# Performance work log

Measured on AMD Instinct MI355X. Metric: run time of the kernel, lower is better.

## Reference

```python
import jax, jax.numpy as jnp
import numpy as np

LATENT, ACTION, HIDDEN, TEMB = 256, 32, 1024, 128
BATCH, NTRAJ, HORIZON = 1024, 16, 5
EPI_W, PRAG_W, CONS_W, GAMMA = 1.0, 1.0, 0.1, 0.99
LOG2PI = float(np.log(2.0 * np.pi))


def _dense_init(key, fan_in, fan_out):
    return jax.random.normal(key, (fan_in, fan_out), dtype=jnp.float32) / np.sqrt(fan_in)


def time_embed(t):
    # sinusoidal embedding, TEMB dims, like ValueNetwork(time_embed_dim=128)
    half = TEMB // 2
    freqs = jnp.exp(-np.log(10000.0) * jnp.arange(half, dtype=jnp.float32) / half)
    ang = t[:, None] * freqs[None, :]  # [B, half]
    return jnp.concatenate([jnp.sin(ang), jnp.cos(ang)], axis=-1)  # [B, TEMB]


def setup_inputs() -> dict:
    key = jax.random.key(0)
    ks = jax.random.split(key, 12)
    return {
        "latent": jax.random.normal(ks[0], (BATCH, LATENT), dtype=jnp.float32),
        "noise": jax.random.normal(ks[1], (NTRAJ, HORIZON, BATCH, ACTION), dtype=jnp.float32),
        # DiffusionConditionedPolicy (state-dependent std): trunk + mean/log_std heads
        "pW1": _dense_init(ks[2], LATENT, HIDDEN), "pb1": jnp.zeros((HIDDEN,), jnp.float32),
        "pW2": _dense_init(ks[3], HIDDEN, HIDDEN), "pb2": jnp.zeros((HIDDEN,), jnp.float32),
        "pWm": _dense_init(ks[4], HIDDEN, ACTION), "pbm": jnp.zeros((ACTION,), jnp.float32),
        "pWs": _dense_init(ks[5], HIDDEN, ACTION), "pbs": jnp.zeros((ACTION,), jnp.float32),
        # LatentDynamicsModel: 3-layer MLP on [latent, action] -> delta
        "dW1": _dense_init(ks[6], LATENT + ACTION, HIDDEN), "db1": jnp.zeros((HIDDEN,), jnp.float32),
        "dW2": _dense_init(ks[7], HIDDEN, HIDDEN), "db2": jnp.zeros((HIDDEN,), jnp.float32),
        "dW3": _dense_init(ks[8], HIDDEN, LATENT), "db3": jnp.zeros((LATENT,), jnp.float32),
        # ValueNetwork: 3-layer MLP on [latent, time_embed] -> scalar
        "vW1": _dense_init(ks[9], LATENT + TEMB, HIDDEN), "vb1": jnp.zeros((HIDDEN,), jnp.float32),
        "vW2": _dense_init(ks[10], HIDDEN, HIDDEN), "vb2": jnp.zeros((HIDDEN,), jnp.float32),
        "vW3": _dense_init(ks[11], HIDDEN, 1), "vb3": jnp.zeros((1,), jnp.float32),
    }


def _efe_forward(latent, noise, pW1, pb1, pW2, pb2, pWm, pbm, pWs, pbs,
                 dW1, db1, dW2, db2, dW3, db3, vW1, vb1, vW2, vb2, vW3, vb3):
    def policy(z, eps):
        h = jax.nn.silu(z @ pW1 + pb1)
        h = jax.nn.silu(h @ pW2 + pb2)
        mean = h @ pWm + pbm
        log_std = jnp.clip(h @ pWs + pbs, -5.0, 2.0)
        action = mean + jnp.exp(log_std) * eps  # reparameterized sample
        # Normal entropy per-dim, summed over action dim
        ent = jnp.sum(0.5 * (1.0 + LOG2PI) + log_std, axis=-1)
        return action, ent

    def dynamics(z, a):
        h = jnp.concatenate([z, a], axis=-1)
        h = jax.nn.silu(h @ dW1 + db1)
        h = jax.nn.silu(h @ dW2 + db2)
        return h @ dW3 + db3  # delta latent

    def value(z, tvec):
        h = jnp.concatenate([z, time_embed(tvec)], axis=-1)
        h = jax.nn.silu(h @ vW1 + vb1)
        h = jax.nn.silu(h @ vW2 + vb2)
        return (h @ vW3 + vb3)[..., 0]  # squeeze(-1)

    def step(z, inp):
        eps_t, t = inp
        action, ent = policy(z, eps_t)
        z_next = z + dynamics(z, action)  # predict_next_latent
        # _compute_latent_kl on normalized latents
        zn = z / (jnp.linalg.norm(z, axis=-1, keepdims=True) + 1e-8)
        pn = z_next / (jnp.linalg.norm(z_next, axis=-1, keepdims=True) + 1e-8)
        kl = 0.5 * jnp.sum((zn - pn) ** 2, axis=-1)
        epistemic = jnp.log1p(kl)
        tvec = jnp.full((z.shape[0],), 0.0, dtype=z.dtype) + t
        pragmatic = value(z_next, tvec)
        consistency = -ent
        step_efe = EPI_W * epistemic + PRAG_W * pragmatic + CONS_W * consistency
        return z_next, step_efe

    ts = jnp.arange(HORIZON, dtype=jnp.float32)

    def rollout(eps_traj):  # eps_traj: [H, B, A]
        _, efes = jax.lax.scan(step, latent, (eps_traj, ts))  # efes: [H, B]
        disc = GAMMA ** ts  # discount_factor ** t
        return jnp.sum(disc[:, None] * efes, axis=0)  # traj_efe: [B]

    traj_efe = jax.vmap(rollout)(noise)  # [NTRAJ, B]
    total_efe = jnp.mean(traj_efe, axis=0)  # sum of traj_efe / num_trajectories
    return total_efe


def reference(latent, noise, pW1, pb1, pW2, pb2, pWm, pbm, pWs, pbs,
              dW1, db1, dW2, db2, dW3, db3, vW1, vb1, vW2, vb2, vW3, vb3):
    return _efe_forward(latent, noise, pW1, pb1, pW2, pb2, pWm, pbm, pWs, pbs,
                        dW1, db1, dW2, db2, dW3, db3, vW1, vb1, vW2, vb2, vW3, vb3)
```

## Files before the change

kernel.cpp:

```cpp
#include <hip/hip_runtime.h>
#include <cstdint>
#include <cstddef>
#include <cmath>


typedef __bf16 bf16;
typedef __attribute__((ext_vector_type(8))) __bf16 bf16x8;
typedef __attribute__((ext_vector_type(4))) __bf16 bf16x4;
typedef __attribute__((ext_vector_type(4))) float f32x4;

static constexpr int BATCH = 1024, NTRAJ = 16, HORIZON = 5;
static constexpr int MR = NTRAJ * BATCH;
static constexpr float ENT_C = 1.4189385332046727f;
static constexpr float SUMDISC = 4.90099501f;

__device__ __forceinline__ void gld_lds16(const bf16* g, const bf16* l) {
  typedef __attribute__((address_space(1))) const uint32_t gq_t;
  typedef __attribute__((address_space(3))) uint32_t lq_t;
  gq_t* gp = (gq_t*)(uintptr_t)g;
  lq_t* lp = (lq_t*)(uint32_t)(uintptr_t)l;
  __builtin_amdgcn_global_load_lds(gp, lp, 16, 0, 0);
}

__device__ __forceinline__ float silu(float x) {
  return x * __builtin_amdgcn_rcpf(1.f + __expf(-x));
}

#define MFMA16(a, b, c) __builtin_amdgcn_mfma_f32_16x16x32_bf16((a), (b), (c), 0, 0, 0)
#define SBAR() __builtin_amdgcn_s_barrier()
#define SCHED0() __builtin_amdgcn_sched_barrier(0)
#define VMCNT(n) asm volatile("s_waitcnt vmcnt(" #n ")" ::: "memory")
#define LGKMCNT0() asm volatile("s_waitcnt lgkmcnt(0)" ::: "memory")

__global__ __launch_bounds__(256) void gemm128(
    const bf16* __restrict__ A, int lda, int K, const bf16* __restrict__ Bt,
    const float* __restrict__ bias, int act_cols,
    bf16* __restrict__ C1, bf16* __restrict__ C2, int ldc) {
  __shared__ alignas(16) bf16 PA[2][2][128 * 32];
  __shared__ alignas(16) bf16 PB[2][2][128 * 32];
  const int tid = threadIdx.x, wave = tid >> 6, lane = tid & 63;
  const int quad = lane >> 4, l16 = lane & 15;
  const int rowBlk = blockIdx.x * 128, colBlk = blockIdx.y * 128;
  const int wr = wave >> 1, wc = wave & 1;
  const int srow = lane >> 2;
  const int skel = (((lane & 3) ^ ((lane >> 3) & 3)) * 8);
  const int qsw = quad ^ ((l16 >> 1) & 3);

  const bf16* gA0 = A + (size_t)(rowBlk + wave * 32 + srow) * lda + skel;
  const bf16* gA1 = gA0 + (size_t)16 * lda;
  const bf16* gB0 = Bt + (size_t)(colBlk + wave * 32 + srow) * K + skel;
  const bf16* gB1 = gB0 + (size_t)16 * K;

#define STG128(t, b)                                      \
  do {                                                    \
    const int k0_ = (t)*64;                               \
    gld_lds16(gA0 + k0_, &PA[b][0][wave * 1024]);         \
    gld_lds16(gA1 + k0_, &PA[b][0][wave * 1024 + 512]);   \
    gld_lds16(gA0 + k0_ + 32, &PA[b][1][wave * 1024]);    \
    gld_lds16(gA1 + k0_ + 32, &PA[b][1][wave * 1024 + 512]); \
    gld_lds16(gB0 + k0_, &PB[b][0][wave * 1024]);         \
    gld_lds16(gB1 + k0_, &PB[b][0][wave * 1024 + 512]);   \
    gld_lds16(gB0 + k0_ + 32, &PB[b][1][wave * 1024]);    \
    gld_lds16(gB1 + k0_ + 32, &PB[b][1][wave * 1024 + 512]); \
  } while (0)

  f32x4 acc[4][4] = {};
  const int nt = K >> 6;
  STG128(0, 0);
  STG128(1, 1);
  VMCNT(8);
  SBAR();
  SCHED0();
  for (int t = 0; t < nt; ++t) {
    const int b = t & 1;
#pragma unroll
    for (int ks = 0; ks < 2; ++ks) {
      const bf16* aRd = &PA[b][ks][(wr * 64 + l16) * 32 + qsw * 8];
      const bf16* bRd = &PB[b][ks][(wc * 64 + l16) * 32 + qsw * 8];
      bf16x8 af[4], bfr[4];
#pragma unroll
      for (int i = 0; i < 4; ++i) {
        af[i] = *(const bf16x8*)(aRd + i * 16 * 32);
        bfr[i] = *(const bf16x8*)(bRd + i * 16 * 32);
      }
#pragma unroll
      for (int mi = 0; mi < 4; ++mi)
#pragma unroll
        for (int ni = 0; ni < 4; ++ni)
          acc[mi][ni] = MFMA16(bfr[ni], af[mi], acc[mi][ni]);
    }
    if (t == nt - 1) break;
    SBAR();
    SCHED0();
    if (t + 2 < nt) {
      STG128(t + 2, b);
      VMCNT(8);
    } else {
      VMCNT(0);
    }
    SBAR();
    SCHED0();
  }
#undef STG128

  const bool doAct = (colBlk < act_cols);
  bf16* const Cp = doAct ? C1 : C2;
  const int cShift = doAct ? 0 : act_cols;
#pragma unroll
  for (int mi = 0; mi < 4; ++mi) {
    const int row = rowBlk + wr * 64 + mi * 16 + l16;
#pragma unroll
    for (int ni = 0; ni < 4; ++ni) {
      const int col0 = colBlk + wc * 64 + ni * 16 + quad * 4;
      const f32x4 bb = *(const f32x4*)(bias + col0);
      bf16x4 o;
#pragma unroll
      for (int r = 0; r < 4; ++r) {
        float x = acc[mi][ni][r] + bb[r];
        if (doAct) x = silu(x);
        o[r] = (bf16)x;
      }
      *(bf16x4*)(Cp + (size_t)row * ldc + (col0 - cShift)) = o;
    }
  }
}

__global__ __launch_bounds__(256) void gemm_pd1v(
    const bf16* __restrict__ A, const bf16* __restrict__ Bt,
    const float* __restrict__ pdb1, const float* __restrict__ vbiasT,
    bf16* __restrict__ Ha, bf16* __restrict__ Hp, bf16* __restrict__ Hv) {
  __shared__ alignas(16) bf16 As0[128 * 32], As1[128 * 32];
  __shared__ alignas(16) bf16 Bs0[128 * 32], Bs1[128 * 32];
  const int tid = threadIdx.x, wave = tid >> 6, lane = tid & 63;
  const int quad = lane >> 4, l16 = lane & 15;
  const int rowBlk = blockIdx.x * 128, colBlk = blockIdx.y * 128;
  const int wr = wave >> 1, wc = wave & 1;
  const int srow = lane >> 2;
  const int skel = (((lane & 3) ^ ((lane >> 3) & 3)) * 8);
  const int qsw = quad ^ ((l16 >> 1) & 3);

  const bf16* gA0 = A + (size_t)(rowBlk + wave * 32 + srow) * 256 + skel;
  const bf16* gA1 = gA0 + (size_t)16 * 256;
  const bf16* gB0 = Bt + (size_t)(colBlk + wave * 32 + srow) * 256 + skel;
  const bf16* gB1 = gB0 + (size_t)16 * 256;
  bf16* const lA0 = As0 + wave * 32 * 32;
  bf16* const lA0b = As0 + (wave * 32 + 16) * 32;
  bf16* const lA1 = As1 + wave * 32 * 32;
  bf16* const lA1b = As1 + (wave * 32 + 16) * 32;
  bf16* const lB0 = Bs0 + wave * 32 * 32;
  bf16* const lB0b = Bs0 + (wave * 32 + 16) * 32;
  bf16* const lB1 = Bs1 + wave * 32 * 32;
  bf16* const lB1b = Bs1 + (wave * 32 + 16) * 32;

  f32x4 acc[4][4] = {};
  for (int k0 = 0; k0 < 256; k0 += 64) {
    gld_lds16(gA0 + k0, lA0);
    gld_lds16(gA1 + k0, lA0b);
    gld_lds16(gA0 + k0 + 32, lA1);
    gld_lds16(gA1 + k0 + 32, lA1b);
    gld_lds16(gB0 + k0, lB0);
    gld_lds16(gB1 + k0, lB0b);
    gld_lds16(gB0 + k0 + 32, lB1);
    gld_lds16(gB1 + k0 + 32, lB1b);
    __syncthreads();
#pragma unroll
    for (int ks = 0; ks < 2; ++ks) {
      const bf16* aRd = (ks ? As1 : As0) + (wr * 64 + l16) * 32 + qsw * 8;
      const bf16* bRd = (ks ? Bs1 : Bs0) + (wc * 64 + l16) * 32 + qsw * 8;
      bf16x8 af[4], bfr[4];
#pragma unroll
      for (int i = 0; i < 4; ++i) {
        af[i] = *(const bf16x8*)(aRd + i * 16 * 32);
        bfr[i] = *(const bf16x8*)(bRd + i * 16 * 32);
      }
#pragma unroll
      for (int mi = 0; mi < 4; ++mi)
#pragma unroll
        for (int ni = 0; ni < 4; ++ni)
          acc[mi][ni] = MFMA16(bfr[ni], af[mi], acc[mi][ni]);
    }
    __syncthreads();
  }

  const int seg = colBlk >> 10;
  bf16* const Cp = (seg == 0) ? Ha : (seg == 1) ? Hp : Hv;
  const int cShift = seg << 10;
  const float* const bp = (seg == 2) ? (vbiasT - 2048) : pdb1;
#pragma unroll
  for (int mi = 0; mi < 4; ++mi) {
    const int row = rowBlk + wr * 64 + mi * 16 + l16;
#pragma unroll
    for (int ni = 0; ni < 4; ++ni) {
      const int col0 = colBlk + wc * 64 + ni * 16 + quad * 4;
      const f32x4 bb = *(const f32x4*)(bp + col0);
      bf16x4 o;
#pragma unroll
      for (int r = 0; r < 4; ++r) {
        float x = acc[mi][ni][r] + bb[r];
        if (seg != 1) x = silu(x);
        o[r] = (bf16)x;
      }
      *(bf16x4*)(Cp + (size_t)row * 1024 + (col0 - cShift)) = o;
    }
  }
}

template <int NT, int EPI>
__device__ __forceinline__ void gemm256_body(
    const bf16* __restrict__ A, const bf16* __restrict__ Bt, int rowBlk,
    int colBlk, const float* __restrict__ bias, const float* __restrict__ aux,
    bf16* __restrict__ C1, float* __restrict__ efe, float disc,
    bf16 (*sAB)[2][256 * 64]) {
  constexpr int K = NT * 64;
  const int tid = threadIdx.x, wave = tid >> 6, lane = tid & 63;
  const int quad = lane >> 4, l16 = lane & 15;
  const int wr = wave >> 2, wc = wave & 3;

  const int j8 = lane >> 3;
  const int c16e = ((lane & 7) ^ j8) * 8;
  const bf16* gAs = A + (size_t)(rowBlk + wave * 16 + j8) * K + c16e;
  const bf16* gBs = Bt + (size_t)(colBlk + wave * 16 + j8) * K + c16e;

#define STAGE_A(hh, tt, bb)                                           \
  do {                                                                \
    const bf16* g_ = gAs + (hh) * 128 * K + (tt) * 64;                \
    bf16* l_ = &sAB[(bb)][0][((hh) * 128 + wave * 16) * 64];          \
    gld_lds16(g_, l_);                                                \
    gld_lds16(g_ + 8 * K, l_ + 8 * 64);                               \
  } while (0)
#define STAGE_B(hh, tt, bb)                                           \
  do {                                                                \
    const bf16* g_ = gBs + (hh) * 128 * K + (tt) * 64;                \
    bf16* l_ = &sAB[(bb)][1][((hh) * 128 + wave * 16) * 64];          \
    gld_lds16(g_, l_);                                                \
    gld_lds16(g_ + 8 * K, l_ + 8 * 64);                               \
  } while (0)

  const int k0x = (quad * 8) ^ ((l16 & 7) << 3);
  const int aOff = (wr * 128 + l16) * 64 + k0x;
  const int bOff = (wc * 64 + l16) * 64 + k0x;

  bf16x8 bAf[4][2], bBf[2][2], bB2f[2][2];
  f32x4 acc[8][4] = {};

  STAGE_A(0, 0, 0);
  STAGE_A(1, 0, 0);
  STAGE_B(0, 0, 0);
  STAGE_B(1, 0, 0);
  STAGE_B(0, 1, 1);
  STAGE_B(1, 1, 1);
  VMCNT(4);
  SBAR();
  SCHED0();

#pragma unroll 2
  for (int t = 0; t < NT; ++t) {
    const int buf = t & 1;
    const bf16* lA = &sAB[buf][0][0];
    const bf16* lB = &sAB[buf][1][0];

#pragma unroll
    for (int m = 0; m < 4; ++m)
#pragma unroll
      for (int ks = 0; ks < 2; ++ks)
        bAf[m][ks] = *(const bf16x8*)(lA + ((aOff + m * 1024) ^ (ks << 5)));
#pragma unroll
    for (int n = 0; n < 2; ++n)
#pragma unroll
      for (int ks = 0; ks < 2; ++ks)
        bBf[n][ks] = *(const bf16x8*)(lB + ((bOff + n * 1024) ^ (ks << 5)));
    if (t + 1 < NT) STAGE_A(0, t + 1, buf ^ 1);
    SBAR();
    LGKMCNT0();
    SCHED0();
    __builtin_amdgcn_s_setprio(1);
#pragma unroll
    for (int ks = 0; ks < 2; ++ks)
#pragma unroll
      for (int m = 0; m < 4; ++m)
#pragma unroll
        for (int n = 0; n < 2; ++n)
          acc[m][n] = MFMA16(bBf[n][ks], bAf[m][ks], acc[m][n]);
    __builtin_amdgcn_s_setprio(0);
    SBAR();
    SCHED0();

#pragma unroll
    for (int n = 0; n < 2; ++n)
#pragma unroll
      for (int ks = 0; ks < 2; ++ks)
        bB2f[n][ks] =
            *(const bf16x8*)(lB + ((bOff + (n + 2) * 1024) ^ (ks << 5)));
    if (t + 1 < NT) STAGE_A(1, t + 1, buf ^ 1);
    SBAR();
    LGKMCNT0();
    SCHED0();
    __builtin_amdgcn_s_setprio(1);
#pragma unroll
    for (int ks = 0; ks < 2; ++ks)
#pragma unroll
      for (int m = 0; m < 4; ++m)
#pragma unroll
        for (int n = 0; n < 2; ++n)
          acc[m][n + 2] = MFMA16(bB2f[n][ks], bAf[m][ks], acc[m][n + 2]);
    __builtin_amdgcn_s_setprio(0);
    SBAR();
    SCHED0();

#pragma unroll
    for (int m = 0; m < 4; ++m)
#pragma unroll
      for (int ks = 0; ks < 2; ++ks)
        bAf[m][ks] =
            *(const bf16x8*)(lA + ((aOff + (m + 4) * 1024) ^ (ks << 5)));
    if (t + 2 < NT) STAGE_B(0, t + 2, buf);
    SBAR();
    LGKMCNT0();
    SCHED0();
    __builtin_amdgcn_s_setprio(1);
#pragma unroll
    for (int ks = 0; ks < 2; ++ks)
#pragma unroll
      for (int m = 0; m < 4; ++m)
#pragma unroll
        for (int n = 0; n < 2; ++n)
          acc[m + 4][n + 2] =
              MFMA16(bB2f[n][ks], bAf[m][ks], acc[m + 4][n + 2]);
    __builtin_amdgcn_s_setprio(0);
    SBAR();
    SCHED0();

    if (t + 2 < NT) STAGE_B(1, t + 2, buf);
    SBAR();
    SCHED0();
    __builtin_amdgcn_s_setprio(1);
#pragma unroll
    for (int ks = 0; ks < 2; ++ks)
#pragma unroll
      for (int m = 0; m < 4; ++m)
#pragma unroll
        for (int n = 0; n < 2; ++n)
          acc[m + 4][n] = MFMA16(bBf[n][ks], bAf[m][ks], acc[m + 4][n]);
    __builtin_amdgcn_s_setprio(0);
    if (t < NT - 2) {
      VMCNT(4);
    } else {
      VMCNT(0);
    }
    SBAR();
    SCHED0();
  }
#undef STAGE_A
#undef STAGE_B

  if constexpr (EPI == 0) {
#pragma unroll
    for (int m = 0; m < 8; ++m) {
      const int row = rowBlk + wr * 128 + m * 16 + l16;
#pragma unroll
      for (int n = 0; n < 4; ++n) {
        const int gcol = colBlk + wc * 64 + n * 16 + quad * 4;
        const f32x4 bb = *(const f32x4*)(bias + gcol);
        bf16x4 o;
#pragma unroll
        for (int r = 0; r < 4; ++r) o[r] = (bf16)silu(acc[m][n][r] + bb[r]);
        *(bf16x4*)(C1 + (size_t)row * 1024 + gcol) = o;
      }
    }
  } else {
#pragma unroll
    for (int m = 0; m < 8; ++m) {
      const int row = rowBlk + wr * 128 + m * 16 + l16;
      float p = 0.f;
#pragma unroll
      for (int n = 0; n < 4; ++n) {
        const int gcol = colBlk + wc * 64 + n * 16 + quad * 4;
        const f32x4 bb = *(const f32x4*)(bias + gcol);
        const f32x4 w3 = *(const f32x4*)(aux + gcol);
#pragma unroll
        for (int r = 0; r < 4; ++r) p += silu(acc[m][n][r] + bb[r]) * w3[r];
      }
      p += __shfl_xor(p, 16);
      p += __shfl_xor(p, 32);
      if (quad == 0) atomicAdd(efe + row, disc * p);
    }
  }
}

template <int NT, int EPI>
__global__ __launch_bounds__(512, 2) void gemm256(
    const bf16* __restrict__ A, const bf16* __restrict__ Bt, int nCol,
    const float* __restrict__ bias, const float* __restrict__ aux,
    bf16* __restrict__ C1, float* __restrict__ efe, float disc) {
  static_assert(NT >= 2, "need at least 2 K-tiles");
  __shared__ alignas(16) bf16 sAB[2][2][256 * 64];
  const int nwg = gridDim.x, flat = blockIdx.x;
  const int lid = (flat & 7) * (nwg >> 3) + (flat >> 3);
  const int rowBlk = (lid / nCol) * 256, colBlk = (lid % nCol) * 256;
  gemm256_body<NT, EPI>(A, Bt, rowBlk, colBlk, bias, aux, C1, efe, disc, sAB);
}

template <int NT>
__global__ __launch_bounds__(512, 2) void gemm256_dual(
    const bf16* __restrict__ A0, const bf16* __restrict__ Bt0,
    const float* __restrict__ bias0, bf16* __restrict__ C0,
    const bf16* __restrict__ A1, const bf16* __restrict__ Bt1,
    const float* __restrict__ bias1, const float* __restrict__ aux1,
    float* __restrict__ efe, float disc) {
  __shared__ alignas(16) bf16 sAB[2][2][256 * 64];
  const int nwg = gridDim.x, flat = blockIdx.x;
  const int lid = (flat & 7) * (nwg >> 3) + (flat >> 3);
  const int job = lid >> 8;
  const int t256 = lid & 255;
  const int rowBlk = (t256 >> 2) * 256, colBlk = (t256 & 3) * 256;
  if (job == 0)
    gemm256_body<NT, 0>(A0, Bt0, rowBlk, colBlk, bias0, nullptr, C0, nullptr,
                        0.f, sAB);
  else
    gemm256_body<NT, 1>(A1, Bt1, rowBlk, colBlk, bias1, aux1, nullptr, efe,
                        disc, sAB);
}

__global__ __launch_bounds__(256) void gemm_dyn3(
    const bf16* __restrict__ A, const bf16* __restrict__ Bt,
    const float* __restrict__ db3, float* __restrict__ Zf,
    bf16* __restrict__ Zb, float* __restrict__ s_n, float* __restrict__ s_c) {
  __shared__ alignas(16) bf16 PA[2][2][64 * 32];
  __shared__ alignas(16) bf16 PB[2][2][128 * 32];
  const int tid = threadIdx.x, wave = tid >> 6, lane = tid & 63;
  const int quad = lane >> 4, l16 = lane & 15;
  const int rowBlk = blockIdx.x * 64, colBlk = blockIdx.y * 128;
  const int srow = lane >> 2;
  const int skel = (((lane & 3) ^ ((lane >> 3) & 3)) * 8);
  const int qsw = quad ^ ((l16 >> 1) & 3);

  const bf16* gA = A + (size_t)(rowBlk + wave * 16 + srow) * 1024 + skel;
  const bf16* gB0 = Bt + (size_t)(colBlk + wave * 32 + srow) * 1024 + skel;
  const bf16* gB1 = gB0 + (size_t)16 * 1024;

#define STGD(t, b)                                        \
  do {                                                    \
    const int k0_ = (t)*64;                               \
    gld_lds16(gA + k0_, &PA[b][0][wave * 512]);           \
    gld_lds16(gA + k0_ + 32, &PA[b][1][wave * 512]);      \
    gld_lds16(gB0 + k0_, &PB[b][0][wave * 1024]);         \
    gld_lds16(gB1 + k0_, &PB[b][0][wave * 1024 + 512]);   \
    gld_lds16(gB0 + k0_ + 32, &PB[b][1][wave * 1024]);    \
    gld_lds16(gB1 + k0_ + 32, &PB[b][1][wave * 1024 + 512]); \
  } while (0)

  f32x4 acc[8] = {};
  STGD(0, 0);
  STGD(1, 1);
  VMCNT(6);
  SBAR();
  SCHED0();
#pragma unroll 2
  for (int t = 0; t < 16; ++t) {
    const int b = t & 1;
#pragma unroll
    for (int ks = 0; ks < 2; ++ks) {
      const bf16* aRd = &PA[b][ks][(wave * 16 + l16) * 32 + qsw * 8];
      const bf16* bRd = &PB[b][ks][l16 * 32 + qsw * 8];
      const bf16x8 af = *(const bf16x8*)aRd;
#pragma unroll
      for (int ni = 0; ni < 8; ++ni) {
        const bf16x8 bfr = *(const bf16x8*)(bRd + ni * 16 * 32);
        acc[ni] = MFMA16(bfr, af, acc[ni]);
      }
    }
    if (t == 15) break;
    SBAR();
    SCHED0();
    if (t < 14) {
      STGD(t + 2, b);
      VMCNT(6);
    } else {
      VMCNT(0);
    }
    SBAR();
    SCHED0();
  }
#undef STGD

  const int row = rowBlk + wave * 16 + l16;
  float pn = 0.f, pc = 0.f;
#pragma unroll
  for (int ni = 0; ni < 8; ++ni) {
    const int col0 = colBlk + ni * 16 + quad * 4;
    const f32x4 b4 = *(const f32x4*)(db3 + col0);
    float* zp = Zf + (size_t)row * 256 + col0;
    const f32x4 z = *(const f32x4*)zp;
    f32x4 zn;
    bf16x4 o;
#pragma unroll
    for (int r = 0; r < 4; ++r) {
      zn[r] = z[r] + acc[ni][r] + b4[r];
      pn += zn[r] * zn[r];
      pc += z[r] * zn[r];
      o[r] = (bf16)zn[r];
    }
    *(f32x4*)zp = zn;
    *(bf16x4*)(Zb + (size_t)row * 256 + col0) = o;
  }
  pn += __shfl_xor(pn, 16);
  pn += __shfl_xor(pn, 32);
  pc += __shfl_xor(pc, 16);
  pc += __shfl_xor(pc, 32);
  if (quad == 0) {
    atomicAdd(s_n + row, pn);
    atomicAdd(s_c + row, pc);
  }
}

__global__ void kl_batch(const float* __restrict__ sz0,
                         const float* __restrict__ snAll,
                         const float* __restrict__ scAll,
                         float* __restrict__ efe) {
  const int m = blockIdx.x * 256 + threadIdx.x;
  float sz = sz0[m];
  float disc = 1.f, acc = 0.f;
  for (int t = 0; t < HORIZON; ++t) {
    const float sn = snAll[t * MR + m], sc = scAll[t * MR + m];
    const float nz = sqrtf(sz) + 1e-8f, nn = sqrtf(sn) + 1e-8f;
    const float kl =
        0.5f * (sz / (nz * nz) + sn / (nn * nn) - 2.f * sc / (nz * nn));
    acc += disc * log1pf(fmaxf(kl, 0.f));
    sz = sn;
    disc *= 0.99f;
  }
  efe[m] += acc;
}

__global__ __launch_bounds__(256) void heads4(
    const bf16* __restrict__ H, const bf16* __restrict__ Wt,
    const float* __restrict__ pbm, const float* __restrict__ pbs,
    const float* __restrict__ noise, const bf16* __restrict__ preD,
    const bf16* __restrict__ dW1at, bf16* __restrict__ Hd,
    float* __restrict__ efe, int t, float disc, int rmask) {
  __shared__ alignas(16) bf16 As[2][4 * 16 * 32];
  __shared__ alignas(16) bf16 Bs[2][4 * 64 * 32];
  __shared__ alignas(16) bf16 LAct[16 * 32];
  const int tid = threadIdx.x, wave = tid >> 6, lane = tid & 63;
  const int quad = lane >> 4, l16 = lane & 15;
  const int rowBlk = blockIdx.x * 16;
  const int srow = lane >> 2;
  const int skel = (((lane & 3) ^ ((lane >> 3) & 3)) * 8);
  const int qsw = quad ^ ((l16 >> 1) & 3);
  const int kw = wave * 256;

  const bf16* gA = H + (size_t)((rowBlk + srow) & rmask) * 1024 + kw + skel;

#define STGH(kt, b)                                                         \
  do {                                                                      \
    gld_lds16(gA + (kt) * 32, &As[b][wave * 512]);                          \
    _Pragma("unroll") for (int j = 0; j < 4; ++j) gld_lds16(                \
        Wt + (size_t)(j * 16 + srow) * 1024 + kw + (kt) * 32 + skel,        \
        &Bs[b][wave * 2048 + j * 512]);                                     \
  } while (0)

  f32x4 acc[4] = {};
  STGH(0, 0);
  STGH(1, 1);
#pragma unroll
  for (int kt = 0; kt < 8; ++kt) {
    const int b = kt & 1;
    if (kt < 7) {
      VMCNT(5);
    } else {
      VMCNT(0);
    }
    SCHED0();
    const bf16x8 af =
        *(const bf16x8*)(&As[b][wave * 512] + l16 * 32 + qsw * 8);
#pragma unroll
    for (int ni = 0; ni < 4; ++ni) {
      const bf16x8 bfr =
          *(const bf16x8*)(&Bs[b][wave * 2048] + (ni * 16 + l16) * 32 + qsw * 8);
      acc[ni] = MFMA16(bfr, af, acc[ni]);
    }
    SCHED0();
    if (kt < 6) {
      LGKMCNT0();
      STGH(kt + 2, b);
    }
  }
#undef STGH

  float* red = (float*)Bs;
#pragma unroll
  for (int ni = 0; ni < 4; ++ni)
    *(f32x4*)(red + wave * 1024 + ni * 256 + lane * 4) = acc[ni];
  __syncthreads();
#pragma unroll
  for (int ni = 0; ni < 4; ++ni) {
    f32x4 s = *(const f32x4*)(red + ni * 256 + lane * 4);
#pragma unroll
    for (int w2 = 1; w2 < 4; ++w2) {
      const f32x4 p = *(const f32x4*)(red + w2 * 1024 + ni * 256 + lane * 4);
#pragma unroll
      for (int r = 0; r < 4; ++r) s[r] += p[r];
    }
    acc[ni] = s;
  }

  const int row = rowBlk + l16;
  const int n = row >> 10, b2 = row & 1023;
  float ent = 0.f;
#pragma unroll
  for (int ni = 0; ni < 2; ++ni) {
    const int col0 = ni * 16 + quad * 4;
    const f32x4 bm4 = *(const f32x4*)(pbm + col0);
    const f32x4 bs4 = *(const f32x4*)(pbs + col0);
    const f32x4 ep4 =
        *(const f32x4*)(noise + (((size_t)(n * 5 + t) * 1024 + b2) * 32 + col0));
    bf16x4 o;
#pragma unroll
    for (int r = 0; r < 4; ++r) {
      const float mean = acc[ni][r] + bm4[r];
      float ls = acc[ni + 2][r] + bs4[r];
      ls = fminf(fmaxf(ls, -5.f), 2.f);
      o[r] = (bf16)(mean + __expf(ls) * ep4[r]);
      ent += ENT_C + ls;
    }
    if (wave == 0) *(bf16x4*)(LAct + l16 * 32 + col0) = o;
  }
  ent += __shfl_xor(ent, 16);
  ent += __shfl_xor(ent, 32);
  if (wave == 0 && quad == 0) efe[row] += disc * (-0.1f) * ent;
  __syncthreads();

  const int prow = row & rmask;
  const bf16x8 af2 = *(const bf16x8*)(LAct + l16 * 32 + quad * 8);
#pragma unroll 4
  for (int ci = 0; ci < 16; ++ci) {
    const int ct = wave * 16 + ci;
    const bf16x8 wf =
        *(const bf16x8*)(dW1at + (size_t)(ct * 16 + l16) * 32 + quad * 8);
    f32x4 a = {};
    a = MFMA16(wf, af2, a);
    const int col0 = ct * 16 + quad * 4;
    const bf16x4 pd = *(const bf16x4*)(preD + (size_t)prow * 1024 + col0);
    bf16x4 o;
#pragma unroll
    for (int r = 0; r < 4; ++r) o[r] = (bf16)silu(a[r] + (float)pd[r]);
    *(bf16x4*)(Hd + (size_t)row * 1024 + col0) = o;
  }
}

__global__ __launch_bounds__(256) void prep_tr(
    const float* __restrict__ pW1, const float* __restrict__ dW1,
    const float* __restrict__ vW1, const float* __restrict__ pW2,
    const float* __restrict__ dW2, const float* __restrict__ dW3,
    const float* __restrict__ vW2, const float* __restrict__ pWm,
    const float* __restrict__ pWs, const float* __restrict__ pb1,
    const float* __restrict__ db1, const float* __restrict__ vb1,
    const float* __restrict__ latent, bf16* __restrict__ pdW1vt,
    bf16* __restrict__ pW2t, bf16* __restrict__ pHt,
    bf16* __restrict__ dW1at, bf16* __restrict__ dW2t,
    bf16* __restrict__ dW3t, bf16* __restrict__ vW2t,
    float* __restrict__ pdb1, float* __restrict__ vbias,
    float* __restrict__ Zf, bf16* __restrict__ Zb0, float* __restrict__ efe,
    float* __restrict__ sz0, float* __restrict__ snAll,
    float* __restrict__ scAll) {
  int bid = blockIdx.x;
  if (bid == 1072) {
    for (int i = threadIdx.x; i < 2048; i += 256)
      pdb1[i] = (i < 1024) ? pb1[i] : db1[i - 1024];
    return;
  }
  if (bid >= 1073 && bid < 1093) {
    const int idx = (bid - 1073) * 256 + threadIdx.x;
    const int t = idx >> 10, j = idx & 1023;
    float s = vb1[j];
    const float lt = (float)t;
    for (int i = 0; i < 64; ++i) {
      const float f = expf(-9.210340371976184f * (float)i / 64.f);
      const float ang = lt * f;
      s += sinf(ang) * vW1[(size_t)(256 + i) * 1024 + j];
      s += cosf(ang) * vW1[(size_t)(256 + 64 + i) * 1024 + j];
    }
    vbias[idx] = s;
    return;
  }
  if (bid >= 1093) {
    const int wave = threadIdx.x >> 6, lane = threadIdx.x & 63;
    const int row = (bid - 1093) * 4 + wave;
    const f32x4 z = *(const f32x4*)(latent + (size_t)(row & 1023) * 256 + lane * 4);
    *(f32x4*)(Zf + (size_t)row * 256 + lane * 4) = z;
    if (row < 1024) {
      bf16x4 o = {(bf16)z[0], (bf16)z[1], (bf16)z[2], (bf16)z[3]};
      *(bf16x4*)(Zb0 + (size_t)row * 256 + lane * 4) = o;
    }
    float s = z[0] * z[0] + z[1] * z[1] + z[2] * z[2] + z[3] * z[3];
#pragma unroll
    for (int m = 1; m < 64; m <<= 1) s += __shfl_xor(s, m);
    if (lane == 0) {
      sz0[row] = s;
      efe[row] = 0.f;
    }
    if (lane < HORIZON) {
      snAll[lane * MR + row] = 0.f;
      scAll[lane * MR + row] = 0.f;
    }
    return;
  }
  const float* in;
  bf16* out;
  int K, N, ldin, ro = 0;
  if (bid < 64) { in = pW1; out = pdW1vt; K = 256; N = 1024; ldin = 1024; }
  else if (bid < 128) { bid -= 64; in = dW1; out = pdW1vt + 1024 * 256; K = 256; N = 1024; ldin = 1024; }
  else if (bid < 192) { bid -= 128; in = vW1; out = pdW1vt + 2048 * 256; K = 256; N = 1024; ldin = 1024; }
  else if (bid < 448) { bid -= 192; in = pW2; out = pW2t; K = 1024; N = 1024; ldin = 1024; }
  else if (bid < 704) { bid -= 448; in = dW2; out = dW2t; K = 1024; N = 1024; ldin = 1024; }
  else if (bid < 960) { bid -= 704; in = vW2; out = vW2t; K = 1024; N = 1024; ldin = 1024; }
  else if (bid < 1024) { bid -= 960; in = dW3; out = dW3t; K = 1024; N = 256; ldin = 256; }
  else if (bid < 1040) { bid -= 1024; in = dW1; out = dW1at; K = 32; N = 1024; ldin = 1024; ro = 256; }
  else if (bid < 1056) { bid -= 1040; in = pWm; out = pHt; K = 1024; N = 32; ldin = 32; }
  else { bid -= 1056; in = pWs; out = pHt + 32 * 1024; K = 1024; N = 32; ldin = 32; }

  const int ktiles = (K + 63) >> 6;
  const int k0 = (bid % ktiles) * 64, n0 = (bid / ktiles) * 64;
  __shared__ float tile[64][65];
  const int tx = threadIdx.x & 63, ty = threadIdx.x >> 6;
#pragma unroll
  for (int i = 0; i < 16; ++i) {
    const int k = k0 + ty + i * 4;
    if (k < K && n0 + tx < N)
      tile[ty + i * 4][tx] = in[(size_t)(ro + k) * ldin + n0 + tx];
  }
  __syncthreads();
#pragma unroll
  for (int i = 0; i < 16; ++i) {
    const int n = n0 + ty + i * 4;
    if (n < N && k0 + tx < K)
      out[(size_t)n * K + k0 + tx] = (bf16)tile[tx][ty + i * 4];
  }
}

__global__ void finalize(const float* __restrict__ efe,
                         const float* __restrict__ vb3,
                         float* __restrict__ out) {
  const int b = blockIdx.x * 256 + threadIdx.x;
  float s = 0.f;
#pragma unroll
  for (int n = 0; n < 16; ++n) s += efe[n * 1024 + b];
  out[b] = s * (1.f / 16.f) + SUMDISC * vb3[0];
}

extern "C" void kernel_launch(void* const* d_in, const int* in_sizes, int n_in,
                              void* d_out, int out_size, void* d_ws,
                              size_t ws_size, hipStream_t stream) {
  const float* latent = (const float*)d_in[0];
  const float* noise = (const float*)d_in[1];
  const float* pW1 = (const float*)d_in[2];
  const float* pb1 = (const float*)d_in[3];
  const float* pW2 = (const float*)d_in[4];
  const float* pb2 = (const float*)d_in[5];
  const float* pWm = (const float*)d_in[6];
  const float* pbm = (const float*)d_in[7];
  const float* pWs = (const float*)d_in[8];
  const float* pbs = (const float*)d_in[9];
  const float* dW1 = (const float*)d_in[10];
  const float* db1 = (const float*)d_in[11];
  const float* dW2 = (const float*)d_in[12];
  const float* db2 = (const float*)d_in[13];
  const float* dW3 = (const float*)d_in[14];
  const float* db3 = (const float*)d_in[15];
  const float* vW1 = (const float*)d_in[16];
  const float* vb1 = (const float*)d_in[17];
  const float* vW2 = (const float*)d_in[18];
  const float* vb2 = (const float*)d_in[19];
  const float* vW3 = (const float*)d_in[20];
  const float* vb3 = (const float*)d_in[21];

  char* w = (char*)d_ws;
  size_t off = 0;
  auto take = [&](size_t bytes) -> void* {
    void* p = (void*)(w + off);
    off = (off + bytes + 255) & ~(size_t)255;
    return p;
  };
  bf16* pdW1vt = (bf16*)take(3072ull * 256 * 2);
  float* pdb1 = (float*)take(2048ull * 4);
  bf16* pW2t = (bf16*)take(1024ull * 1024 * 2);
  bf16* pHt = (bf16*)take(64ull * 1024 * 2);
  bf16* dW1at = (bf16*)take(1024ull * 32 * 2);
  bf16* dW2t = (bf16*)take(1024ull * 1024 * 2);
  bf16* dW3t = (bf16*)take(256ull * 1024 * 2);
  bf16* vW2t = (bf16*)take(1024ull * 1024 * 2);
  float* vbias = (float*)take(5ull * 1024 * 4);
  bf16* Zb0 = (bf16*)take(1024ull * 256 * 2);
  bf16* Zb = (bf16*)take((size_t)MR * 256 * 2);
  float* Zf = (float*)take((size_t)MR * 256 * 4);
  float* efe = (float*)take((size_t)MR * 4);
  float* sz0 = (float*)take((size_t)MR * 4);
  float* snAll = (float*)take(5ull * MR * 4);
  float* scAll = (float*)take(5ull * MR * 4);
  bf16* Ha = (bf16*)take((size_t)MR * 1024 * 2);
  bf16* Hc = (bf16*)take((size_t)MR * 1024 * 2);
  bf16* Hp = (bf16*)take((size_t)MR * 1024 * 2);
  bf16* Hv = (bf16*)take((size_t)MR * 1024 * 2);
  bf16* vW1t = pdW1vt + (size_t)2048 * 256;

  const dim3 blk(256), blk2(512);
  const int BIG = 1 << 30;
  prep_tr<<<dim3(1093 + MR / 4), blk, 0, stream>>>(
      pW1, dW1, vW1, pW2, dW2, dW3, vW2, pWm, pWs, pb1, db1, vb1, latent,
      pdW1vt, pW2t, pHt, dW1at, dW2t, dW3t, vW2t, pdb1, vbias, Zf, Zb0, efe,
      sz0, snAll, scAll);

  float disc = 1.f, dprev = 1.f;
  for (int s = 0; s < HORIZON; ++s) {
    const int rmask = (s == 0) ? 1023 : 0x7FFFFFFF;
    if (s == 0) {
      gemm128<<<dim3(8, 16), blk, 0, stream>>>(Zb0, 256, 256, pdW1vt, pdb1,
                                               1024, Ha, Hp, 1024);
      gemm128<<<dim3(8, 8), blk, 0, stream>>>(Ha, 1024, 1024, pW2t, pb2, BIG,
                                              Hc, Hc, 1024);
    } else {
      gemm_pd1v<<<dim3(128, 24), blk, 0, stream>>>(
          Zb, pdW1vt, pdb1, vbias + (s - 1) * 1024, Ha, Hp, Hv);
      gemm256_dual<16><<<dim3(512), blk2, 0, stream>>>(
          Ha, pW2t, pb2, Hc, Hv, vW2t, vb2, vW3, efe, dprev);
    }
    heads4<<<dim3(MR / 16), blk, 0, stream>>>(Hc, pHt, pbm, pbs, noise, Hp,
                                              dW1at, Ha, efe, s, disc, rmask);
    gemm256<16, 0><<<dim3(256), blk2, 0, stream>>>(Ha, dW2t, 4, db2, nullptr,
                                                   Hc, nullptr, 0.f);
    gemm_dyn3<<<dim3(MR / 64, 2), blk, 0, stream>>>(
        Hc, dW3t, db3, Zf, Zb, snAll + (size_t)s * MR, scAll + (size_t)s * MR);
    dprev = disc;
    disc *= 0.99f;
  }

  kl_batch<<<dim3(MR / 256), blk, 0, stream>>>(sz0, snAll, scAll, efe);

  gemm128<<<dim3(128, 8), blk, 0, stream>>>(Zb, 256, 256, vW1t,
                                            vbias + 4 * 1024, BIG, Hv, Hv,
                                            1024);
  gemm256<16, 1><<<dim3(256), blk2, 0, stream>>>(Hv, vW2t, 4, vb2, vW3,
                                                 nullptr, efe, dprev);
  finalize<<<dim3(4), blk, 0, stream>>>(efe, vb3, (float*)d_out);
}
```

Baseline: 1.045 ms.

## Retile fused first-layer GEMM to 256x256 blocks and reorder dual-GEMM block mapping

Replaces the 128x128 first-layer GEMM (policy/dynamics/value layer 1, K=256) with a 512-thread 256x256 tile kernel that loads the full K-tile of 64 at once with XOR-swizzled LDS. The same kernel is reused for the final value layer-1 GEMM, with the bias pointer arranged so that all output goes to Hv. The aim is more data reuse per block and fewer blocks. The dual GEMM's block-to-job mapping is also changed to interleave the two jobs in groups of eight blocks. The larger tiles raise register and LDS pressure and leave fewer blocks to fill the GPU.

```diff
diff --git a/kernel.cpp b/kernel.cpp
--- a/kernel.cpp
+++ b/kernel.cpp
@@ -125,59 +125,58 @@
   }
 }
 
-__global__ __launch_bounds__(256) void gemm_pd1v(
+__global__ __launch_bounds__(512, 2) void gemm_pd1v256(
     const bf16* __restrict__ A, const bf16* __restrict__ Bt,
     const float* __restrict__ pdb1, const float* __restrict__ vbiasT,
     bf16* __restrict__ Ha, bf16* __restrict__ Hp, bf16* __restrict__ Hv) {
-  __shared__ alignas(16) bf16 As0[128 * 32], As1[128 * 32];
-  __shared__ alignas(16) bf16 Bs0[128 * 32], Bs1[128 * 32];
+  __shared__ alignas(16) bf16 sA[256 * 64], sB[256 * 64];
   const int tid = threadIdx.x, wave = tid >> 6, lane = tid & 63;
   const int quad = lane >> 4, l16 = lane & 15;
-  const int rowBlk = blockIdx.x * 128, colBlk = blockIdx.y * 128;
-  const int wr = wave >> 1, wc = wave & 1;
-  const int srow = lane >> 2;
-  const int skel = (((lane & 3) ^ ((lane >> 3) & 3)) * 8);
-  const int qsw = quad ^ ((l16 >> 1) & 3);
-
-  const bf16* gA0 = A + (size_t)(rowBlk + wave * 32 + srow) * 256 + skel;
-  const bf16* gA1 = gA0 + (size_t)16 * 256;
-  const bf16* gB0 = Bt + (size_t)(colBlk + wave * 32 + srow) * 256 + skel;
-  const bf16* gB1 = gB0 + (size_t)16 * 256;
-  bf16* const lA0 = As0 + wave * 32 * 32;
-  bf16* const lA0b = As0 + (wave * 32 + 16) * 32;
-  bf16* const lA1 = As1 + wave * 32 * 32;
-  bf16* const lA1b = As1 + (wave * 32 + 16) * 32;
-  bf16* const lB0 = Bs0 + wave * 32 * 32;
-  bf16* const lB0b = Bs0 + (wave * 32 + 16) * 32;
-  bf16* const lB1 = Bs1 + wave * 32 * 32;
-  bf16* const lB1b = Bs1 + (wave * 32 + 16) * 32;
-
-  f32x4 acc[4][4] = {};
-  for (int k0 = 0; k0 < 256; k0 += 64) {
-    gld_lds16(gA0 + k0, lA0);
-    gld_lds16(gA1 + k0, lA0b);
-    gld_lds16(gA0 + k0 + 32, lA1);
-    gld_lds16(gA1 + k0 + 32, lA1b);
-    gld_lds16(gB0 + k0, lB0);
-    gld_lds16(gB1 + k0, lB0b);
-    gld_lds16(gB0 + k0 + 32, lB1);
-    gld_lds16(gB1 + k0 + 32, lB1b);
+  const int wr = wave >> 2, wc = wave & 3;
+  const int rowBlk = blockIdx.x * 256, colBlk = blockIdx.y * 256;
+
+  const int j8 = lane >> 3;
+  const int c16e = ((lane & 7) ^ j8) * 8;
+  const bf16* gAs = A + (size_t)(rowBlk + wave * 16 + j8) * 256 + c16e;
+  const bf16* gBs = Bt + (size_t)(colBlk + wave * 16 + j8) * 256 + c16e;
+
+  const int k0x = (quad * 8) ^ ((l16 & 7) << 3);
+  const int aOff = (wr * 128 + l16) * 64 + k0x;
+  const int bOff = (wc * 64 + l16) * 64 + k0x;
+
+  f32x4 acc[8][4] = {};
+#pragma unroll
+  for (int t = 0; t < 4; ++t) {
+    const int kk = t * 64;
+    {
+      const bf16* g0 = gAs + kk;
+      bf16* l0 = &sA[wave * 16 * 64];
+      gld_lds16(g0, l0);
+      gld_lds16(g0 + 8 * 256, l0 + 8 * 64);
+      gld_lds16(g0 + 128 * 256, l0 + 128 * 64);
+      gld_lds16(g0 + 136 * 256, l0 + 136 * 64);
+      const bf16* g1 = gBs + kk;
+      bf16* l1 = &sB[wave * 16 * 64];
+      gld_lds16(g1, l1);
+      gld_lds16(g1 + 8 * 256, l1 + 8 * 64);
+      gld_lds16(g1 + 128 * 256, l1 + 128 * 64);
+      gld_lds16(g1 + 136 * 256, l1 + 136 * 64);
+    }
     __syncthreads();
 #pragma unroll
     for (int ks = 0; ks < 2; ++ks) {
-      const bf16* aRd = (ks ? As1 : As0) + (wr * 64 + l16) * 32 + qsw * 8;
-      const bf16* bRd = (ks ? Bs1 : Bs0) + (wc * 64 + l16) * 32 + qsw * 8;
-      bf16x8 af[4], bfr[4];
-#pragma unroll
-      for (int i = 0; i < 4; ++i) {
-        af[i] = *(const bf16x8*)(aRd + i * 16 * 32);
-        bfr[i] = *(const bf16x8*)(bRd + i * 16 * 32);
-      }
-#pragma unroll
-      for (int mi = 0; mi < 4; ++mi)
-#pragma unroll
-        for (int ni = 0; ni < 4; ++ni)
-          acc[mi][ni] = MFMA16(bfr[ni], af[mi], acc[mi][ni]);
+      bf16x8 af[8], bfr[4];
+#pragma unroll
+      for (int m = 0; m < 8; ++m)
+        af[m] = *(const bf16x8*)(&sA[0] + ((aOff + m * 1024) ^ (ks << 5)));
+#pragma unroll
+      for (int n = 0; n < 4; ++n)
+        bfr[n] = *(const bf16x8*)(&sB[0] + ((bOff + n * 1024) ^ (ks << 5)));
+#pragma unroll
+      for (int m = 0; m < 8; ++m)
+#pragma unroll
+        for (int n = 0; n < 4; ++n)
+          acc[m][n] = MFMA16(bfr[n], af[m], acc[m][n]);
     }
     __syncthreads();
   }
@@ -187,16 +186,16 @@
   const int cShift = seg << 10;
   const float* const bp = (seg == 2) ? (vbiasT - 2048) : pdb1;
 #pragma unroll
-  for (int mi = 0; mi < 4; ++mi) {
-    const int row = rowBlk + wr * 64 + mi * 16 + l16;
-#pragma unroll
-    for (int ni = 0; ni < 4; ++ni) {
-      const int col0 = colBlk + wc * 64 + ni * 16 + quad * 4;
+  for (int m = 0; m < 8; ++m) {
+    const int row = rowBlk + wr * 128 + m * 16 + l16;
+#pragma unroll
+    for (int n = 0; n < 4; ++n) {
+      const int col0 = colBlk + wc * 64 + n * 16 + quad * 4;
       const f32x4 bb = *(const f32x4*)(bp + col0);
       bf16x4 o;
 #pragma unroll
       for (int r = 0; r < 4; ++r) {
-        float x = acc[mi][ni][r] + bb[r];
+        float x = acc[m][n][r] + bb[r];
         if (seg != 1) x = silu(x);
         o[r] = (bf16)x;
       }
@@ -408,11 +407,10 @@
     const float* __restrict__ bias1, const float* __restrict__ aux1,
     float* __restrict__ efe, float disc) {
   __shared__ alignas(16) bf16 sAB[2][2][256 * 64];
-  const int nwg = gridDim.x, flat = blockIdx.x;
-  const int lid = (flat & 7) * (nwg >> 3) + (flat >> 3);
-  const int job = lid >> 8;
-  const int t256 = lid & 255;
-  const int rowBlk = (t256 >> 2) * 256, colBlk = (t256 & 3) * 256;
+  const int flat = blockIdx.x;
+  const int job = (flat >> 3) & 1;
+  const int seq = (flat & 7) * 32 + (flat >> 4);
+  const int rowBlk = (seq >> 2) * 256, colBlk = (seq & 3) * 256;
   if (job == 0)
     gemm256_body<NT, 0>(A0, Bt0, rowBlk, colBlk, bias0, nullptr, C0, nullptr,
                         0.f, sAB);
@@ -819,7 +817,7 @@
       gemm128<<<dim3(8, 8), blk, 0, stream>>>(Ha, 1024, 1024, pW2t, pb2, BIG,
                                               Hc, Hc, 1024);
     } else {
-      gemm_pd1v<<<dim3(128, 24), blk, 0, stream>>>(
+      gemm_pd1v256<<<dim3(64, 12), blk2, 0, stream>>>(
           Zb, pdW1vt, pdb1, vbias + (s - 1) * 1024, Ha, Hp, Hv);
       gemm256_dual<16><<<dim3(512), blk2, 0, stream>>>(
           Ha, pW2t, pb2, Hc, Hv, vW2t, vb2, vW3, efe, dprev);
@@ -836,9 +834,8 @@
 
   kl_batch<<<dim3(MR / 256), blk, 0, stream>>>(sz0, snAll, scAll, efe);
 
-  gemm128<<<dim3(128, 8), blk, 0, stream>>>(Zb, 256, 256, vW1t,
-                                            vbias + 4 * 1024, BIG, Hv, Hv,
-                                            1024);
+  gemm_pd1v256<<<dim3(64, 4), blk2, 0, stream>>>(
+      Zb, vW1t, vbias + 4 * 1024, vbias, Hv, Hv, Hv);
   gemm256<16, 1><<<dim3(256), blk2, 0, stream>>>(Hv, vW2t, 4, vb2, vW3,
                                                  nullptr, efe, dprev);
   finalize<<<dim3(4), blk, 0, stream>>>(efe, vb3, (float*)d_out);
```

Result: no change. 1.064 ms (+1.8%).
